# Optimization experiments

Measured on AMD Instinct MI355X. Metric: run time of the kernel, lower is better.

## Reference

```python
import jax, jax.numpy as jnp
import numpy as np

N, F_IN, F_OUT = 8192, 512, 256
NEG_BIG = -9e15


def setup_inputs() -> dict:
    key = jax.random.key(0)
    k1, k2, k3, k4, k5 = jax.random.split(key, 5)
    h = jax.random.normal(k1, (N, F_IN), dtype=jnp.float32)
    adj = jax.random.randint(k2, (N, N), 0, 2, dtype=jnp.int32)
    W = jax.random.normal(k3, (F_IN, F_OUT), dtype=jnp.float32) / np.sqrt(F_IN)
    bW = jnp.zeros((F_OUT,), dtype=jnp.float32)
    a1 = jax.random.normal(k4, (F_OUT,), dtype=jnp.float32) / np.sqrt(2 * F_OUT)
    a2 = jax.random.normal(k5, (F_OUT,), dtype=jnp.float32) / np.sqrt(2 * F_OUT)
    ba = jnp.zeros((), dtype=jnp.float32)
    return {"h": h, "adj": adj, "W": W, "bW": bW, "a1": a1, "a2": a2, "ba": ba}


def reference(h, adj, W, bW, a1, a2, ba):
    # Wh: [N, F_OUT]
    Wh = h @ W + bW
    # a([Wh_i ; Wh_j]) + b == (Wh_i . a1) + (Wh_j . a2) + b  (rank-1 decomposition,
    # avoids the O(N^2 * 2F) repeat/cat tensor the torch code materializes)
    f1 = Wh @ a1  # [N]
    f2 = Wh @ a2  # [N]
    e = jax.nn.leaky_relu(f1[:, None] + f2[None, :] + ba, negative_slope=0.2)
    e = jnp.where(adj > 0, e, NEG_BIG)
    attention = jax.nn.softmax(e, axis=1)  # dropout = identity (eval mode)
    return attention @ Wh
```

## Files before the change

### kernel.cpp

```cpp
#include <hip/hip_runtime.h>

typedef __bf16 bf16;
typedef __attribute__((ext_vector_type(4))) float f32x4;
typedef __attribute__((ext_vector_type(8))) __bf16 bf16x8;
typedef __attribute__((ext_vector_type(4))) __bf16 bf16x4;
typedef __attribute__((ext_vector_type(4))) int i32x4;

#define NN 8192
#define FI 512
#define FO 256
#define NSPLIT 4
#define JCHUNK (NN / NSPLIT)

__global__ __launch_bounds__(256) void kw_split(const float* __restrict__ W,
                                                bf16* __restrict__ wth,
                                                bf16* __restrict__ wtl) {
  const int idx = blockIdx.x * 256 + threadIdx.x;
  const int k = idx >> 8, n = idx & 255;
  float x = W[idx];
  bf16 hi = (bf16)x;
  wth[(size_t)n * FI + k] = hi;
  wtl[(size_t)n * FI + k] = (bf16)(x - (float)hi);
}

__global__ __launch_bounds__(256) void k1_gemm(
    const float* __restrict__ h, const bf16* __restrict__ wth,
    const bf16* __restrict__ wtl, const float* __restrict__ bW,
    const float* __restrict__ a1, const float* __restrict__ a2,
    bf16* __restrict__ whb, float* __restrict__ f1, float* __restrict__ f2) {
  __shared__ bf16 Ah[32 * 40];
  __shared__ bf16 Al[32 * 40];
  const int t = threadIdx.x;
  const int lane = t & 63, w = t >> 6;
  const int m16 = lane & 15, q = lane >> 4;
  const int bi = blockIdx.x, bj = blockIdx.y;
  const int i0 = bi * 32;
  const int n0 = bj * 128 + w * 32;
  const int srow = t >> 3, skoff = (t & 7) * 4;

  const f32x4 z4 = {0.f, 0.f, 0.f, 0.f};
  f32x4 acc[2][2];
#pragma unroll
  for (int mt = 0; mt < 2; ++mt)
#pragma unroll
    for (int nt = 0; nt < 2; ++nt) acc[mt][nt] = z4;

  const float* hrow = h + (size_t)(i0 + srow) * FI + skoff;

  for (int kt = 0; kt < FI / 32; ++kt) {
    f32x4 hv = *(const f32x4*)(hrow + kt * 32);
    bf16x8 bh[2], bl[2];
#pragma unroll
    for (int nt = 0; nt < 2; ++nt) {
      const size_t woff = (size_t)(n0 + nt * 16 + m16) * FI + kt * 32 + q * 8;
      bh[nt] = *(const bf16x8*)(wth + woff);
      bl[nt] = *(const bf16x8*)(wtl + woff);
    }
    bf16x4 hh, hl;
#pragma unroll
    for (int x = 0; x < 4; ++x) {
      float v = hv[x];
      bf16 hi = (bf16)v;
      hh[x] = hi;
      hl[x] = (bf16)(v - (float)hi);
    }
    __syncthreads();
    *(bf16x4*)&Ah[srow * 40 + skoff] = hh;
    *(bf16x4*)&Al[srow * 40 + skoff] = hl;
    __syncthreads();
#pragma unroll
    for (int mt = 0; mt < 2; ++mt) {
      bf16x8 ah = *(const bf16x8*)&Ah[(mt * 16 + m16) * 40 + q * 8];
      bf16x8 al = *(const bf16x8*)&Al[(mt * 16 + m16) * 40 + q * 8];
#pragma unroll
      for (int nt = 0; nt < 2; ++nt) {
        acc[mt][nt] = __builtin_amdgcn_mfma_f32_16x16x32_bf16(ah, bh[nt], acc[mt][nt], 0, 0, 0);
        acc[mt][nt] = __builtin_amdgcn_mfma_f32_16x16x32_bf16(al, bh[nt], acc[mt][nt], 0, 0, 0);
        acc[mt][nt] = __builtin_amdgcn_mfma_f32_16x16x32_bf16(ah, bl[nt], acc[mt][nt], 0, 0, 0);
      }
    }
  }
  float f1p[2][4] = {}, f2p[2][4] = {};
#pragma unroll
  for (int nt = 0; nt < 2; ++nt) {
    const int n = n0 + nt * 16 + m16;
    const float bw = bW[n], av1 = a1[n], av2 = a2[n];
#pragma unroll
    for (int mt = 0; mt < 2; ++mt) {
#pragma unroll
      for (int reg = 0; reg < 4; ++reg) {
        float wh = acc[mt][nt][reg] + bw;
        const int il = mt * 16 + q * 4 + reg;
        whb[(size_t)bi * (FO * 32) + n * 32 + il] = (bf16)wh;
        f1p[mt][reg] += wh * av1;
        f2p[mt][reg] += wh * av2;
      }
    }
  }
#pragma unroll
  for (int m = 1; m < 16; m <<= 1) {
#pragma unroll
    for (int mt = 0; mt < 2; ++mt)
#pragma unroll
      for (int reg = 0; reg < 4; ++reg) {
        f1p[mt][reg] += __shfl_xor(f1p[mt][reg], m);
        f2p[mt][reg] += __shfl_xor(f2p[mt][reg], m);
      }
  }
  if (m16 == 0) {
#pragma unroll
    for (int mt = 0; mt < 2; ++mt)
#pragma unroll
      for (int reg = 0; reg < 4; ++reg) {
        const int i = i0 + mt * 16 + q * 4 + reg;
        atomicAdd(&f1[i], f1p[mt][reg]);
        atomicAdd(&f2[i], f2p[mt][reg]);
      }
  }
}

__global__ __launch_bounds__(256, 4) void k4_attn(
    const int* __restrict__ adj, const bf16* __restrict__ whb,
    const float* __restrict__ f1, const float* __restrict__ f2,
    const float* __restrict__ ba_p,
    float* __restrict__ acc_part, float* __restrict__ l_part) {
  __shared__ bf16 Pl[32 * 40];
  const int t = threadIdx.x;
  const int lane = t & 63, w = t >> 6;
  const int m16 = lane & 15, q = lane >> 4;
  const int rb = blockIdx.x, s = blockIdx.y;
  const int i0 = rb * 32;
  const int rloc = t >> 3;
  const int jj = (t & 7) * 4;

  const float ba = *ba_p;
  const float ci = f1[i0 + rloc] + ba;
  const float arg0 = ci + 8.0f;
  const float sh = fmaxf(arg0, 0.2f * arg0);

  const f32x4 z4 = {0.f, 0.f, 0.f, 0.f};
  f32x4 acc[2][4];
#pragma unroll
  for (int mt = 0; mt < 2; ++mt)
#pragma unroll
    for (int cc = 0; cc < 4; ++cc) acc[mt][cc] = z4;
  float lreg = 0.f;

  const int sbase = s * JCHUNK;
  const int* arow = adj + (size_t)(i0 + rloc) * NN + sbase + jj;
  const float* frow = f2 + sbase + jj;

  for (int kt = 0; kt < JCHUNK / 32; ++kt) {
    i32x4 av = *(const i32x4*)(arow + kt * 32);
    f32x4 s4 = *(const f32x4*)(frow + kt * 32);
    const size_t bbase = (size_t)((sbase + kt * 32) >> 5) * (FO * 32) + q * 8;
    bf16x8 bfr[4];
#pragma unroll
    for (int cc = 0; cc < 4; ++cc)
      bfr[cc] = *(const bf16x8*)(whb + bbase + (size_t)((w * 4 + cc) * 16 + m16) * 32);
    float pv[4];
#pragma unroll
    for (int x = 0; x < 4; ++x) {
      float arg = ci + s4[x];
      float e = fmaxf(arg, 0.2f * arg);
      pv[x] = (av[x] > 0) ? __expf(e - sh) : 0.f;
    }
#pragma unroll
    for (int x = 0; x < 4; ++x) lreg += pv[x];
    __syncthreads();
    bf16x4 pb;
#pragma unroll
    for (int x = 0; x < 4; ++x) pb[x] = (bf16)pv[x];
    *(bf16x4*)&Pl[rloc * 40 + jj] = pb;
    __syncthreads();
#pragma unroll
    for (int mt = 0; mt < 2; ++mt) {
      bf16x8 af = *(const bf16x8*)&Pl[(mt * 16 + m16) * 40 + q * 8];
#pragma unroll
      for (int cc = 0; cc < 4; ++cc)
        acc[mt][cc] = __builtin_amdgcn_mfma_f32_16x16x32_bf16(af, bfr[cc], acc[mt][cc], 0, 0, 0);
    }
  }
  lreg += __shfl_xor(lreg, 1);
  lreg += __shfl_xor(lreg, 2);
  lreg += __shfl_xor(lreg, 4);
  if ((t & 7) == 0) l_part[(size_t)s * NN + i0 + rloc] = lreg;
  float* ap = acc_part + (size_t)s * ((size_t)NN * FO);
#pragma unroll
  for (int mt = 0; mt < 2; ++mt) {
#pragma unroll
    for (int cc = 0; cc < 4; ++cc) {
      const int n = (w * 4 + cc) * 16 + m16;
#pragma unroll
      for (int reg = 0; reg < 4; ++reg) {
        const int r = i0 + mt * 16 + q * 4 + reg;
        ap[(size_t)r * FO + n] = acc[mt][cc][reg];
      }
    }
  }
}

__global__ __launch_bounds__(256) void k5_reduce(
    const float* __restrict__ accp, const float* __restrict__ lp,
    float* __restrict__ out) {
  const int idx = blockIdx.x * 256 + threadIdx.x;
  const int i = idx >> 6, n4 = (idx & 63) * 4;
  f32x4 sum = {0.f, 0.f, 0.f, 0.f};
  float l = 0.f;
#pragma unroll
  for (int s = 0; s < NSPLIT; ++s) {
    sum += *(const f32x4*)&accp[(size_t)s * ((size_t)NN * FO) + (size_t)i * FO + n4];
    l += lp[s * NN + i];
  }
  const float rl = 1.0f / l;
  f32x4 o = sum * rl;
  *(f32x4*)&out[(size_t)i * FO + n4] = o;
}

extern "C" void kernel_launch(void* const* d_in, const int* in_sizes, int n_in,
                              void* d_out, int out_size, void* d_ws, size_t ws_size,
                              hipStream_t stream) {
  const float* h   = (const float*)d_in[0];
  const int*   adj = (const int*)d_in[1];
  const float* W   = (const float*)d_in[2];
  const float* bW  = (const float*)d_in[3];
  const float* a1  = (const float*)d_in[4];
  const float* a2  = (const float*)d_in[5];
  const float* ba  = (const float*)d_in[6];
  float* out = (float*)d_out;

  char* ws = (char*)d_ws;
  bf16* whb   = (bf16*)ws;
  float* f1   = (float*)(ws + 4u * 1024 * 1024);
  float* f2   = (float*)(ws + 4u * 1024 * 1024 + 32 * 1024);
  float* accp = (float*)(ws + 4u * 1024 * 1024 + 64 * 1024);
  float* lp   = accp + (size_t)NSPLIT * NN * FO;
  bf16* wth   = (bf16*)((char*)lp + (size_t)NSPLIT * NN * 4);
  bf16* wtl   = wth + (size_t)FO * FI;

  hipMemsetAsync(f1, 0, 64 * 1024, stream);

  kw_split<<<FI * FO / 256, 256, 0, stream>>>(W, wth, wtl);
  k1_gemm<<<dim3(NN / 32, 2), 256, 0, stream>>>(h, wth, wtl, bW, a1, a2, whb, f1, f2);
  k4_attn<<<dim3(NN / 32, NSPLIT), 256, 0, stream>>>(adj, whb, f1, f2, ba, accp, lp);
  k5_reduce<<<(NN * FO / 4) / 256, 256, 0, stream>>>(accp, lp, out);
}
```

Before: 483.7 us.

## Load MFMA A-operands directly into registers and drop LDS staging in GEMM and attention

Both the projection GEMM and the attention kernel now have each wave compute its MFMA A fragment (the h split or the probability values) directly in registers, for a 16-row by 128-column tile. This removes the per-iteration LDS round trip and the two __syncthreads barriers. The attention kernel also prefetches the next adjacency and f2 tile one iteration ahead. The GEMM stages its output tile in LDS so it can write Wh back with coalesced 16-byte stores, and it launches one block per 32 rows instead of two. In exchange, adjacency is loaded redundantly (each row is read by both column-half waves), and accumulator register pressure goes up.

```diff
diff --git a/kernel.cpp b/kernel.cpp
--- a/kernel.cpp
+++ b/kernel.cpp
@@ -28,95 +28,84 @@
     const bf16* __restrict__ wtl, const float* __restrict__ bW,
     const float* __restrict__ a1, const float* __restrict__ a2,
     bf16* __restrict__ whb, float* __restrict__ f1, float* __restrict__ f2) {
-  __shared__ bf16 Ah[32 * 40];
-  __shared__ bf16 Al[32 * 40];
+  __shared__ bf16 stg[32 * 256];
   const int t = threadIdx.x;
   const int lane = t & 63, w = t >> 6;
   const int m16 = lane & 15, q = lane >> 4;
-  const int bi = blockIdx.x, bj = blockIdx.y;
-  const int i0 = bi * 32;
-  const int n0 = bj * 128 + w * 32;
-  const int srow = t >> 3, skoff = (t & 7) * 4;
+  const int wr = w & 1, wn = w >> 1;
+  const int rb = blockIdx.x;
+  const int row = rb * 32 + wr * 16 + m16;
+  const int nb = wn * 128;
 
   const f32x4 z4 = {0.f, 0.f, 0.f, 0.f};
-  f32x4 acc[2][2];
-#pragma unroll
-  for (int mt = 0; mt < 2; ++mt)
-#pragma unroll
-    for (int nt = 0; nt < 2; ++nt) acc[mt][nt] = z4;
-
-  const float* hrow = h + (size_t)(i0 + srow) * FI + skoff;
+  f32x4 acc[8];
+#pragma unroll
+  for (int nn = 0; nn < 8; ++nn) acc[nn] = z4;
+
+  const float* hrow = h + (size_t)row * FI + q * 8;
+  const bf16* wthp = wth + (size_t)(nb + m16) * FI + q * 8;
+  const bf16* wtlp = wtl + (size_t)(nb + m16) * FI + q * 8;
 
   for (int kt = 0; kt < FI / 32; ++kt) {
-    f32x4 hv = *(const f32x4*)(hrow + kt * 32);
-    bf16x8 bh[2], bl[2];
-#pragma unroll
-    for (int nt = 0; nt < 2; ++nt) {
-      const size_t woff = (size_t)(n0 + nt * 16 + m16) * FI + kt * 32 + q * 8;
-      bh[nt] = *(const bf16x8*)(wth + woff);
-      bl[nt] = *(const bf16x8*)(wtl + woff);
-    }
-    bf16x4 hh, hl;
+    f32x4 h0 = *(const f32x4*)(hrow + kt * 32);
+    f32x4 h1 = *(const f32x4*)(hrow + kt * 32 + 4);
+    bf16x8 hh, hl;
 #pragma unroll
     for (int x = 0; x < 4; ++x) {
-      float v = hv[x];
+      float v = h0[x];
       bf16 hi = (bf16)v;
       hh[x] = hi;
       hl[x] = (bf16)(v - (float)hi);
-    }
-    __syncthreads();
-    *(bf16x4*)&Ah[srow * 40 + skoff] = hh;
-    *(bf16x4*)&Al[srow * 40 + skoff] = hl;
-    __syncthreads();
-#pragma unroll
-    for (int mt = 0; mt < 2; ++mt) {
-      bf16x8 ah = *(const bf16x8*)&Ah[(mt * 16 + m16) * 40 + q * 8];
-      bf16x8 al = *(const bf16x8*)&Al[(mt * 16 + m16) * 40 + q * 8];
-#pragma unroll
-      for (int nt = 0; nt < 2; ++nt) {
-        acc[mt][nt] = __builtin_amdgcn_mfma_f32_16x16x32_bf16(ah, bh[nt], acc[mt][nt], 0, 0, 0);
-        acc[mt][nt] = __builtin_amdgcn_mfma_f32_16x16x32_bf16(al, bh[nt], acc[mt][nt], 0, 0, 0);
-        acc[mt][nt] = __builtin_amdgcn_mfma_f32_16x16x32_bf16(ah, bl[nt], acc[mt][nt], 0, 0, 0);
-      }
-    }
-  }
-  float f1p[2][4] = {}, f2p[2][4] = {};
-#pragma unroll
-  for (int nt = 0; nt < 2; ++nt) {
-    const int n = n0 + nt * 16 + m16;
+      float v2 = h1[x];
+      bf16 hi2 = (bf16)v2;
+      hh[4 + x] = hi2;
+      hl[4 + x] = (bf16)(v2 - (float)hi2);
+    }
+#pragma unroll
+    for (int nn = 0; nn < 8; ++nn) {
+      const size_t woff = (size_t)(nn * 16) * FI + kt * 32;
+      bf16x8 bh = *(const bf16x8*)(wthp + woff);
+      bf16x8 bl = *(const bf16x8*)(wtlp + woff);
+      acc[nn] = __builtin_amdgcn_mfma_f32_16x16x32_bf16(hh, bh, acc[nn], 0, 0, 0);
+      acc[nn] = __builtin_amdgcn_mfma_f32_16x16x32_bf16(hl, bh, acc[nn], 0, 0, 0);
+      acc[nn] = __builtin_amdgcn_mfma_f32_16x16x32_bf16(hh, bl, acc[nn], 0, 0, 0);
+    }
+  }
+  float f1p[4] = {}, f2p[4] = {};
+  const int il = wr * 16 + q * 4;
+#pragma unroll
+  for (int nn = 0; nn < 8; ++nn) {
+    const int n = nb + nn * 16 + m16;
     const float bw = bW[n], av1 = a1[n], av2 = a2[n];
 #pragma unroll
-    for (int mt = 0; mt < 2; ++mt) {
-#pragma unroll
-      for (int reg = 0; reg < 4; ++reg) {
-        float wh = acc[mt][nt][reg] + bw;
-        const int il = mt * 16 + q * 4 + reg;
-        whb[(size_t)bi * (FO * 32) + n * 32 + il] = (bf16)wh;
-        f1p[mt][reg] += wh * av1;
-        f2p[mt][reg] += wh * av2;
-      }
+    for (int reg = 0; reg < 4; ++reg) {
+      float wh = acc[nn][reg] + bw;
+      stg[n * 32 + il + reg] = (bf16)wh;
+      f1p[reg] += wh * av1;
+      f2p[reg] += wh * av2;
     }
   }
 #pragma unroll
   for (int m = 1; m < 16; m <<= 1) {
 #pragma unroll
-    for (int mt = 0; mt < 2; ++mt)
-#pragma unroll
-      for (int reg = 0; reg < 4; ++reg) {
-        f1p[mt][reg] += __shfl_xor(f1p[mt][reg], m);
-        f2p[mt][reg] += __shfl_xor(f2p[mt][reg], m);
-      }
+    for (int reg = 0; reg < 4; ++reg) {
+      f1p[reg] += __shfl_xor(f1p[reg], m);
+      f2p[reg] += __shfl_xor(f2p[reg], m);
+    }
   }
   if (m16 == 0) {
 #pragma unroll
-    for (int mt = 0; mt < 2; ++mt)
-#pragma unroll
-      for (int reg = 0; reg < 4; ++reg) {
-        const int i = i0 + mt * 16 + q * 4 + reg;
-        atomicAdd(&f1[i], f1p[mt][reg]);
-        atomicAdd(&f2[i], f2p[mt][reg]);
-      }
-  }
+    for (int reg = 0; reg < 4; ++reg) {
+      const int i = rb * 32 + wr * 16 + q * 4 + reg;
+      atomicAdd(&f1[i], f1p[reg]);
+      atomicAdd(&f2[i], f2p[reg]);
+    }
+  }
+  __syncthreads();
+  bf16x8* dst = (bf16x8*)(whb + (size_t)rb * (FO * 32));
+  const bf16x8* srcv = (const bf16x8*)stg;
+#pragma unroll
+  for (int u = 0; u < 4; ++u) dst[t * 4 + u] = srcv[t * 4 + u];
 }
 
 __global__ __launch_bounds__(256, 4) void k4_attn(
@@ -124,78 +113,82 @@
     const float* __restrict__ f1, const float* __restrict__ f2,
     const float* __restrict__ ba_p,
     float* __restrict__ acc_part, float* __restrict__ l_part) {
-  __shared__ bf16 Pl[32 * 40];
   const int t = threadIdx.x;
   const int lane = t & 63, w = t >> 6;
   const int m16 = lane & 15, q = lane >> 4;
+  const int wr = w & 1, wn = w >> 1;
   const int rb = blockIdx.x, s = blockIdx.y;
   const int i0 = rb * 32;
-  const int rloc = t >> 3;
-  const int jj = (t & 7) * 4;
+  const int row = i0 + wr * 16 + m16;
 
   const float ba = *ba_p;
-  const float ci = f1[i0 + rloc] + ba;
+  const float ci = f1[row] + ba;
   const float arg0 = ci + 8.0f;
   const float sh = fmaxf(arg0, 0.2f * arg0);
 
   const f32x4 z4 = {0.f, 0.f, 0.f, 0.f};
-  f32x4 acc[2][4];
-#pragma unroll
-  for (int mt = 0; mt < 2; ++mt)
-#pragma unroll
-    for (int cc = 0; cc < 4; ++cc) acc[mt][cc] = z4;
+  f32x4 acc[8];
+#pragma unroll
+  for (int nn = 0; nn < 8; ++nn) acc[nn] = z4;
   float lreg = 0.f;
 
   const int sbase = s * JCHUNK;
-  const int* arow = adj + (size_t)(i0 + rloc) * NN + sbase + jj;
-  const float* frow = f2 + sbase + jj;
-
-  for (int kt = 0; kt < JCHUNK / 32; ++kt) {
-    i32x4 av = *(const i32x4*)(arow + kt * 32);
-    f32x4 s4 = *(const f32x4*)(frow + kt * 32);
-    const size_t bbase = (size_t)((sbase + kt * 32) >> 5) * (FO * 32) + q * 8;
-    bf16x8 bfr[4];
-#pragma unroll
-    for (int cc = 0; cc < 4; ++cc)
-      bfr[cc] = *(const bf16x8*)(whb + bbase + (size_t)((w * 4 + cc) * 16 + m16) * 32);
-    float pv[4];
+  const int* arow = adj + (size_t)row * NN + sbase + q * 8;
+  const float* frow = f2 + sbase + q * 8;
+  const bf16* bptr = whb + (size_t)(sbase >> 5) * (FO * 32) +
+                     (size_t)(wn * 128 + m16) * 32 + q * 8;
+
+  i32x4 na0 = *(const i32x4*)(arow);
+  i32x4 na1 = *(const i32x4*)(arow + 4);
+  f32x4 nf0 = *(const f32x4*)(frow);
+  f32x4 nf1 = *(const f32x4*)(frow + 4);
+
+  const int KT = JCHUNK / 32;
+  for (int kt = 0; kt < KT; ++kt) {
+    const i32x4 ca0 = na0;
+    const i32x4 ca1 = na1;
+    const f32x4 cf0 = nf0;
+    const f32x4 cf1 = nf1;
+    if (kt + 1 < KT) {
+      na0 = *(const i32x4*)(arow + (kt + 1) * 32);
+      na1 = *(const i32x4*)(arow + (kt + 1) * 32 + 4);
+      nf0 = *(const f32x4*)(frow + (kt + 1) * 32);
+      nf1 = *(const f32x4*)(frow + (kt + 1) * 32 + 4);
+    }
+    float pv[8];
 #pragma unroll
     for (int x = 0; x < 4; ++x) {
-      float arg = ci + s4[x];
+      float arg = ci + cf0[x];
       float e = fmaxf(arg, 0.2f * arg);
-      pv[x] = (av[x] > 0) ? __expf(e - sh) : 0.f;
-    }
-#pragma unroll
-    for (int x = 0; x < 4; ++x) lreg += pv[x];
-    __syncthreads();
-    bf16x4 pb;
-#pragma unroll
-    for (int x = 0; x < 4; ++x) pb[x] = (bf16)pv[x];
-    *(bf16x4*)&Pl[rloc * 40 + jj] = pb;
-    __syncthreads();
-#pragma unroll
-    for (int mt = 0; mt < 2; ++mt) {
-      bf16x8 af = *(const bf16x8*)&Pl[(mt * 16 + m16) * 40 + q * 8];
-#pragma unroll
-      for (int cc = 0; cc < 4; ++cc)
-        acc[mt][cc] = __builtin_amdgcn_mfma_f32_16x16x32_bf16(af, bfr[cc], acc[mt][cc], 0, 0, 0);
-    }
-  }
-  lreg += __shfl_xor(lreg, 1);
-  lreg += __shfl_xor(lreg, 2);
-  lreg += __shfl_xor(lreg, 4);
-  if ((t & 7) == 0) l_part[(size_t)s * NN + i0 + rloc] = lreg;
+      pv[x] = (ca0[x] > 0) ? __expf(e - sh) : 0.f;
+      float arg2 = ci + cf1[x];
+      float e2 = fmaxf(arg2, 0.2f * arg2);
+      pv[4 + x] = (ca1[x] > 0) ? __expf(e2 - sh) : 0.f;
+    }
+    bf16x8 af;
+#pragma unroll
+    for (int x = 0; x < 8; ++x) {
+      lreg += pv[x];
+      af[x] = (bf16)pv[x];
+    }
+    const bf16* bk = bptr + (size_t)kt * (FO * 32);
+#pragma unroll
+    for (int nn = 0; nn < 8; ++nn) {
+      bf16x8 bfr = *(const bf16x8*)(bk + nn * (16 * 32));
+      acc[nn] = __builtin_amdgcn_mfma_f32_16x16x32_bf16(af, bfr, acc[nn], 0, 0, 0);
+    }
+  }
+  lreg += __shfl_xor(lreg, 16);
+  lreg += __shfl_xor(lreg, 32);
+  if (q == 0 && wn == 0) l_part[(size_t)s * NN + row] = lreg;
   float* ap = acc_part + (size_t)s * ((size_t)NN * FO);
-#pragma unroll
-  for (int mt = 0; mt < 2; ++mt) {
-#pragma unroll
-    for (int cc = 0; cc < 4; ++cc) {
-      const int n = (w * 4 + cc) * 16 + m16;
-#pragma unroll
-      for (int reg = 0; reg < 4; ++reg) {
-        const int r = i0 + mt * 16 + q * 4 + reg;
-        ap[(size_t)r * FO + n] = acc[mt][cc][reg];
-      }
+  const int r0 = i0 + wr * 16 + q * 4;
+#pragma unroll
+  for (int nn = 0; nn < 8; ++nn) {
+    const int n = wn * 128 + nn * 16 + m16;
+#pragma unroll
+    for (int reg = 0; reg < 4; ++reg) {
+      ap[(size_t)(r0 + reg) * FO + n] = acc[nn][reg];
     }
   }
 }
@@ -241,7 +234,7 @@
   hipMemsetAsync(f1, 0, 64 * 1024, stream);
 
   kw_split<<<FI * FO / 256, 256, 0, stream>>>(W, wth, wtl);
-  k1_gemm<<<dim3(NN / 32, 2), 256, 0, stream>>>(h, wth, wtl, bW, a1, a2, whb, f1, f2);
+  k1_gemm<<<NN / 32, 256, 0, stream>>>(h, wth, wtl, bW, a1, a2, whb, f1, f2);
   k4_attn<<<dim3(NN / 32, NSPLIT), 256, 0, stream>>>(adj, whb, f1, f2, ba, accp, lp);
   k5_reduce<<<(NN * FO / 4) / 256, 256, 0, stream>>>(accp, lp, out);
 }
```

Measured after the change: 569.5 us. 1.18x slower.
